# Kernel tuning notes

Measured on AMD Instinct MI355X. Metric: run time of the kernel, lower is better.

Reference implementation:

```python
import jax, jax.numpy as jnp
import numpy as np

B, L, U, H = 16, 1024, 512, 2  # batch, seq_len, units, highway_num


def setup_inputs() -> dict:
    key = jax.random.key(0)
    ks = jax.random.split(key, 8)
    s = 0.02  # weight init scale
    return {
        "inputs": jax.random.normal(ks[0], (B, L, U), dtype=jnp.float32),
        "tW": jax.random.normal(ks[1], (H, U, U), dtype=jnp.float32) * s,
        "tb": jnp.zeros((H, U), dtype=jnp.float32),
        "cW": jax.random.normal(ks[2], (H, U, U), dtype=jnp.float32) * s,
        "cb": jnp.zeros((H, U), dtype=jnp.float32),
        "aW": jax.random.normal(ks[3], (3 * U,), dtype=jnp.float32) * s,
        "ab": jnp.zeros((1,), dtype=jnp.float32),
        "frW": jax.random.normal(ks[4], (2 * U, U), dtype=jnp.float32) * s,
        "frb": jnp.zeros((U,), dtype=jnp.float32),
        "ffW": jax.random.normal(ks[5], (2 * U, U), dtype=jnp.float32) * s,
        "ffb": jnp.zeros((U,), dtype=jnp.float32),
    }


def reference(inputs, tW, tb, cW, cb, aW, ab, frW, frb, ffW, ffb):
    # Highway stack (inference: dropout is identity)
    x = inputs
    for i in range(tW.shape[0]):
        t = jax.nn.relu(x @ tW[i] + tb[i])
        c = jax.nn.sigmoid(x @ cW[i] + cb[i])
        x = t * c + x * (1.0 - c)

    # Pairwise MLP self-attention.
    # Original: A_ij = relu(dense1(concat([x_i, x_j, x_i*x_j]))).
    # Split aW = [w1; w2; w3] so we never materialize the [B,L,L,3U] tensor:
    # A_ij = relu(x_i.w1 + x_j.w2 + sum_d x_i_d * x_j_d * w3_d + b)
    u = x.shape[-1]
    w1, w2, w3 = aW[:u], aW[u:2 * u], aW[2 * u:]
    s1 = x @ w1                                    # [B,L]
    s2 = x @ w2                                    # [B,L]
    s3 = jnp.einsum('bid,bjd->bij', x * w3, x)     # [B,L,L]
    A = jax.nn.relu(s1[:, :, None] + s2[:, None, :] + s3 + ab[0])
    att = jnp.einsum('bij,bjd->bid', jax.nn.softmax(A, axis=-1), x)

    # Fuse gate. NOTE: original code uses fuse_f_dense (sigmoid) for BOTH
    # z and f (fuse_z_dense is never called), so z == f at inference.
    concat = jnp.concatenate([inputs, att], axis=-1)  # [B,L,2U]
    z = jax.nn.sigmoid(concat @ ffW + ffb)
    r = jax.nn.sigmoid(concat @ frW + frb)
    f = z
    return r * inputs + f * z
```

## Files before the change

kernel.cpp:

```cpp
#include <hip/hip_runtime.h>
#include <math.h>

typedef __bf16 bf16;
typedef __attribute__((ext_vector_type(8))) __bf16 bf16x8;
typedef __attribute__((ext_vector_type(4))) float f32x4;


__device__ __forceinline__ void load_lds16(const bf16* g, bf16* l) {
  __builtin_amdgcn_global_load_lds(
      (const __attribute__((address_space(1))) unsigned int*)(g),
      (__attribute__((address_space(3))) unsigned int*)(l), 16, 0, 0);
}

struct DualArgs {
  const bf16* A; const bf16* A2;
  const bf16* Bt;
  void* C; const void* xres;
  const float* bias_t; const float* bias_c;
  int K, ldb;
  const float* aW;
  float* s1a; float* s2a;
  bf16* q;
  bf16* xT;
};

template<int EPI>
__global__ __launch_bounds__(256, 4)
void gemm_dual(DualArgs g) {
  __shared__ bf16 smem[2 * 128 * 64];
  bf16* As = smem;
  bf16* Bs = smem + 8192;
  const int tid = threadIdx.x;
  const int bid = blockIdx.x;
  const int xcd = bid & 7;
  const int t = bid >> 3;
  const int bx = t & 7;
  const int r  = t >> 3;
  const int Rx = gridDim.x >> 6;
  const int by = xcd * Rx + r;

  const int wid = tid >> 6, lane = tid & 63;
  const int wm = (wid >> 1) << 6;
  const int wn = (wid & 1) << 6;
  const int lr = lane & 15, lq = lane >> 4;

  f32x4 acc[4][4];
#pragma unroll
  for (int i = 0; i < 4; i++)
#pragma unroll
    for (int j = 0; j < 4; j++) acc[i][j] = f32x4{0.f, 0.f, 0.f, 0.f};

  const int srow8 = (tid >> 3) & 7;
  const int skc   = (tid & 7) ^ srow8;
  const int lswz  = (lr & 7);
  const long long abase = (long long)(by * 128) * 512;

  for (int k0 = 0; k0 < g.K; k0 += 64) {
    const bf16* Ak = (k0 < 512) ? g.A : g.A2;
    const int kk = k0 & 511;
    __syncthreads();
#pragma unroll
    for (int j = 0; j < 4; j++) {
      const int ci = (tid >> 6) * 4 + j;
      const int bn = ci * 8 + srow8;
      load_lds16(Ak + abase + (long long)bn * 512 + kk + skc * 8, As + ci * 512);
      const int grp = bn >> 5, r5 = bn & 31;
      const int grow = ((grp & 1) << 9) + bx * 64 + ((grp >> 1) << 5) + r5;
      load_lds16(g.Bt + (long long)grow * g.ldb + k0 + skc * 8, Bs + ci * 512);
    }
    __syncthreads();
#pragma unroll
    for (int ks = 0; ks < 2; ks++) {
      bf16x8 af[4], bfr[4];
      const int kx = (ks * 4 + lq) ^ lswz;
#pragma unroll
      for (int i = 0; i < 4; i++)
        af[i] = *(const bf16x8*)(&As[(wm + i * 16 + lr) * 64 + kx * 8]);
#pragma unroll
      for (int j = 0; j < 4; j++)
        bfr[j] = *(const bf16x8*)(&Bs[(wn + j * 16 + lr) * 64 + kx * 8]);
#pragma unroll
      for (int i = 0; i < 4; i++)
#pragma unroll
        for (int j = 0; j < 4; j++)
          acc[i][j] = __builtin_amdgcn_mfma_f32_16x16x32_bf16(af[i], bfr[j], acc[i][j], 0, 0, 0);
    }
  }

  const int colb = bx * 64 + (wn >> 1);
  bf16 xn_arr[4][4][2];
#pragma unroll
  for (int i = 0; i < 4; i++) {
#pragma unroll
    for (int v = 0; v < 4; v++) {
      int row = by * 128 + wm + i * 16 + lq * 4 + v;
      float p1s = 0.f, p2s = 0.f;
#pragma unroll
      for (int j = 0; j < 2; j++) {
        int col = colb + j * 16 + lr;
        long long idx = (long long)row * 512 + col;
        float p0 = acc[i][j][v] + g.bias_t[col];
        float p1 = acc[i][j + 2][v] + g.bias_c[col];
        if (EPI == 1) {
          float z = 1.f / (1.f + __expf(-p0));
          float rr = 1.f / (1.f + __expf(-p1));
          float x = (float)((const bf16*)g.xres)[idx];
          ((float*)g.C)[idx] = rr * x + z * z;
        } else {
          float tt = fmaxf(p0, 0.f);
          float c = 1.f / (1.f + __expf(-p1));
          float x = (float)((const bf16*)g.xres)[idx];
          bf16 xn = (bf16)(tt * c + x * (1.f - c));
          ((bf16*)g.C)[idx] = xn;
          if (EPI == 2) {
            xn_arr[i][v][j] = xn;
            float xf = (float)xn;
            p1s += xf * g.aW[col];
            p2s += xf * g.aW[512 + col];
            g.q[idx] = (bf16)(xf * g.aW[1024 + col]);
          }
        }
      }
      if (EPI == 2) {
        p1s += __shfl_xor(p1s, 1, 64);
        p1s += __shfl_xor(p1s, 2, 64);
        p1s += __shfl_xor(p1s, 4, 64);
        p1s += __shfl_xor(p1s, 8, 64);
        p2s += __shfl_xor(p2s, 1, 64);
        p2s += __shfl_xor(p2s, 2, 64);
        p2s += __shfl_xor(p2s, 4, 64);
        p2s += __shfl_xor(p2s, 8, 64);
        if (lr == 0) {
          atomicAdd(&g.s1a[row], p1s);
          atomicAdd(&g.s2a[row], p2s);
        }
      }
    }
  }

  if (EPI == 2) {
    bf16* Ts = smem;
    __syncthreads();
#pragma unroll
    for (int i = 0; i < 4; i++)
#pragma unroll
      for (int v = 0; v < 4; v++)
#pragma unroll
        for (int j = 0; j < 2; j++) {
          int rloc = wm + i * 16 + lq * 4 + v;
          int cloc = (wn >> 1) + j * 16 + lr;
          Ts[cloc * 136 + rloc] = xn_arr[i][v][j];
        }
    __syncthreads();
    const int b = by >> 3;
    bf16* dst = g.xT + (long long)b * 524288 + ((by & 7) * 128);
#pragma unroll
    for (int it = 0; it < 2; it++) {
      int d = (tid >> 3) + it * 32;
      int jb = (tid & 7) * 16;
      bf16x8 v0 = *(const bf16x8*)(&Ts[d * 136 + jb]);
      bf16x8 v1 = *(const bf16x8*)(&Ts[d * 136 + jb + 8]);
      long long o = (long long)(bx * 64 + d) * 1024 + jb;
      *(bf16x8*)(dst + o) = v0;
      *(bf16x8*)(dst + o + 8) = v1;
    }
  }
}

struct AttnArgs {
  const bf16* Q;
  const bf16* X;
  const bf16* XT;
  bf16* O;
  const float* s1; const float* s2; const float* abp;
};

__global__ __launch_bounds__(512, 2)
void attn_fused(AttnArgs g) {
  __shared__ __align__(16) bf16 smem[57344];
  __shared__ float lsum_sh[4][64];
  bf16* Qs = smem;
  bf16* Es = smem + 49152;
  const int tid = threadIdx.x;
  const int bid = blockIdx.x;
  const int gr = (bid & 7) * 32 + (bid >> 3);
  const int bz = gr >> 4, qt = gr & 15;
  const int wid = tid >> 6, lane = tid & 63;
  const int wr = wid >> 2, wc = wid & 3;
  const int lr = lane & 15, lq = lane >> 4;
  const int lswz = lr & 7;
  const int srow8 = (lane >> 3) & 7;
  const int skc = (lane & 7) ^ srow8;

  const bf16* Qg = g.Q + (long long)bz * 524288 + (long long)(qt * 64) * 512;
  const bf16* Xg = g.X + (long long)bz * 524288;
  const bf16* XTg = g.XT + (long long)bz * 524288;

#pragma unroll
  for (int c8 = 0; c8 < 8; c8++) {
    const int row = c8 * 8 + srow8;
    load_lds16(Qg + (long long)row * 512 + wid * 64 + skc * 8,
               Qs + (wid * 8 + c8) * 512);
  }
#pragma unroll
  for (int jj = 0; jj < 2; jj++) {
    const int c = wid * 2 + jj;
    load_lds16(Xg + (long long)(c * 8 + srow8) * 512 + skc * 8,
               smem + 32768 + c * 512);
  }

  float s1r[2][4];
#pragma unroll
  for (int i = 0; i < 2; i++)
#pragma unroll
    for (int v = 0; v < 4; v++)
      s1r[i][v] = g.s1[bz * 1024 + qt * 64 + wr * 32 + i * 16 + lq * 4 + v] + g.abp[0];

  f32x4 acc_o[2][8];
  float lsum[2][4];
#pragma unroll
  for (int i = 0; i < 2; i++) {
#pragma unroll
    for (int jd = 0; jd < 8; jd++) acc_o[i][jd] = f32x4{0.f, 0.f, 0.f, 0.f};
#pragma unroll
    for (int v = 0; v < 4; v++) lsum[i][v] = 0.f;
  }

  __syncthreads();

  int cur = 0;
  for (int jt = 0; jt < 8; jt++) {
    f32x4 acc_s[2][2];
#pragma unroll
    for (int i = 0; i < 2; i++)
#pragma unroll
      for (int jjf = 0; jjf < 2; jjf++) acc_s[i][jjf] = f32x4{0.f, 0.f, 0.f, 0.f};

    for (int p = 0; p < 8; p++) {
      if (p < 7) {
#pragma unroll
        for (int jj = 0; jj < 2; jj++) {
          const int c = wid * 2 + jj;
          load_lds16(Xg + (long long)(jt * 128 + c * 8 + srow8) * 512 + (p + 1) * 64 + skc * 8,
                     smem + 32768 + (cur ^ 1) * 8192 + c * 512);
        }
      } else if (jt + 1 < 8) {
#pragma unroll
        for (int jj = 0; jj < 2; jj++) {
          const int c = wid * 2 + jj;
          load_lds16(Xg + (long long)((jt + 1) * 128 + c * 8 + srow8) * 512 + skc * 8,
                     smem + 32768 + (cur ^ 1) * 8192 + c * 512);
        }
      }
      bf16x8 aq[2][2], bx[2][2];
#pragma unroll
      for (int ks = 0; ks < 2; ks++) {
        const int kx = (ks * 4 + lq) ^ lswz;
#pragma unroll
        for (int i = 0; i < 2; i++)
          aq[i][ks] = *(const bf16x8*)(&Qs[p * 4096 + (wr * 32 + i * 16 + lr) * 64 + kx * 8]);
#pragma unroll
        for (int jjf = 0; jjf < 2; jjf++)
          bx[jjf][ks] = *(const bf16x8*)(&smem[32768 + cur * 8192 + (wc * 32 + jjf * 16 + lr) * 64 + kx * 8]);
      }
#pragma unroll
      for (int i = 0; i < 2; i++)
#pragma unroll
        for (int jjf = 0; jjf < 2; jjf++)
#pragma unroll
          for (int ks = 0; ks < 2; ks++)
            acc_s[i][jjf] = __builtin_amdgcn_mfma_f32_16x16x32_bf16(aq[i][ks], bx[jjf][ks], acc_s[i][jjf], 0, 0, 0);
      __syncthreads();
      cur ^= 1;
    }

    float s2v[2];
#pragma unroll
    for (int jjf = 0; jjf < 2; jjf++)
      s2v[jjf] = g.s2[bz * 1024 + jt * 128 + wc * 32 + jjf * 16 + lr];
#pragma unroll
    for (int i = 0; i < 2; i++) {
#pragma unroll
      for (int v = 0; v < 4; v++) {
        const int rl = wr * 32 + i * 16 + lq * 4 + v;
        float ps = 0.f;
#pragma unroll
        for (int jjf = 0; jjf < 2; jjf++) {
          const int jl = wc * 32 + jjf * 16 + lr;
          float val = acc_s[i][jjf][v] + s1r[i][v] + s2v[jjf];
          val = fminf(fmaxf(val, 0.f), 60.f);
          val = __expf(val);
          bf16 eb = (bf16)val;
          ps += (float)eb;
          Es[(jl >> 6) * 4096 + rl * 64 + (((jl >> 3) & 7) ^ (rl & 7)) * 8 + (jl & 7)] = eb;
        }
        ps += __shfl_xor(ps, 1, 64);
        ps += __shfl_xor(ps, 2, 64);
        ps += __shfl_xor(ps, 4, 64);
        ps += __shfl_xor(ps, 8, 64);
        lsum[i][v] += ps;
      }
    }
    __syncthreads();

#pragma unroll
    for (int kq = 0; kq < 4; kq++) {
      bf16x8 aE[2];
      const int kx = (((kq & 1) * 4 + lq)) ^ lswz;
#pragma unroll
      for (int i = 0; i < 2; i++)
        aE[i] = *(const bf16x8*)(&Es[(kq >> 1) * 4096 + (wr * 32 + i * 16 + lr) * 64 + kx * 8]);
      bf16x8 bv[8];
#pragma unroll
      for (int jd = 0; jd < 8; jd++)
        bv[jd] = *(const bf16x8*)(XTg + (long long)(wc * 128 + jd * 16 + lr) * 1024
                                  + jt * 128 + kq * 32 + lq * 8);
#pragma unroll
      for (int jd = 0; jd < 8; jd++) {
        acc_o[0][jd] = __builtin_amdgcn_mfma_f32_16x16x32_bf16(aE[0], bv[jd], acc_o[0][jd], 0, 0, 0);
        acc_o[1][jd] = __builtin_amdgcn_mfma_f32_16x16x32_bf16(aE[1], bv[jd], acc_o[1][jd], 0, 0, 0);
      }
    }
  }

  if (lr == 0) {
#pragma unroll
    for (int i = 0; i < 2; i++)
#pragma unroll
      for (int v = 0; v < 4; v++)
        lsum_sh[wc][wr * 32 + i * 16 + lq * 4 + v] = lsum[i][v];
  }
  __syncthreads();

  bf16* Ts = smem;
  float rinv[2][4];
#pragma unroll
  for (int i = 0; i < 2; i++)
#pragma unroll
    for (int v = 0; v < 4; v++) {
      const int rl = wr * 32 + i * 16 + lq * 4 + v;
      const float tot = lsum_sh[0][rl] + lsum_sh[1][rl] + lsum_sh[2][rl] + lsum_sh[3][rl];
      rinv[i][v] = 1.f / tot;
    }
  __syncthreads();
#pragma unroll
  for (int i = 0; i < 2; i++)
#pragma unroll
    for (int jd = 0; jd < 8; jd++)
#pragma unroll
      for (int v = 0; v < 4; v++) {
        const int rl = wr * 32 + i * 16 + lq * 4 + v;
        const int d = wc * 128 + jd * 16 + lr;
        Ts[rl * 520 + d] = (bf16)(acc_o[i][jd][v] * rinv[i][v]);
      }
  __syncthreads();
  bf16* Og = g.O + (long long)bz * 524288 + (long long)(qt * 64) * 512;
#pragma unroll
  for (int rr = 0; rr < 8; rr++) {
    const int row = wid * 8 + rr;
    bf16x8 vv = *(const bf16x8*)(&Ts[row * 520 + lane * 8]);
    *(bf16x8*)(Og + (long long)row * 512 + lane * 8) = vv;
  }
}

__device__ __forceinline__ void tile_transpose(const float* src, int sld,
                                               bf16* dst, int dld,
                                               int k0, int n0, int tid) {
  __shared__ float tile[64][65];
  const int rr = tid >> 4, c4 = (tid & 15) * 4;
#pragma unroll
  for (int it = 0; it < 4; it++) {
    int r = rr + it * 16;
    f32x4 v = *(const f32x4*)(src + (long long)(k0 + r) * sld + n0 + c4);
    tile[r][c4] = v[0]; tile[r][c4 + 1] = v[1];
    tile[r][c4 + 2] = v[2]; tile[r][c4 + 3] = v[3];
  }
  __syncthreads();
  const int nl = tid >> 2, kb = (tid & 3) * 16;
  bf16x8 o0, o1;
#pragma unroll
  for (int kk = 0; kk < 8; kk++) o0[kk] = (bf16)tile[kb + kk][nl];
#pragma unroll
  for (int kk = 0; kk < 8; kk++) o1[kk] = (bf16)tile[kb + 8 + kk][nl];
  bf16* d = dst + (long long)(n0 + nl) * dld + k0 + kb;
  *(bf16x8*)d = o0;
  *(bf16x8*)(d + 8) = o1;
}

__global__ void prep(const float* tW, const float* tb, const float* cW, const float* cb,
                     const float* frW, const float* frb, const float* ffW, const float* ffb,
                     const float* inp, bf16* xb0,
                     bf16* w1T, bf16* w2T, float* bias1, float* bias2, float* sred) {
  const int bid = blockIdx.x, tid = threadIdx.x;
  if (bid < 256) {
    const int quad = bid >> 6, tile = bid & 63;
    const int l = quad >> 1, half = quad & 1;
    const float* src = (half ? cW : tW) + l * 262144;
    bf16* dst = w1T + l * 524288 + half * 262144;
    tile_transpose(src, 512, dst, 512, (tile >> 3) * 64, (tile & 7) * 64, tid);
  } else if (bid < 512) {
    const int j = bid - 256;
    const int half = j >> 7, tile = j & 127;
    const float* src = half ? frW : ffW;
    bf16* dst = w2T + half * 524288;
    tile_transpose(src, 512, dst, 1024, (tile >> 3) * 64, (tile & 7) * 64, tid);
  } else if (bid < 4608) {
    long long i8 = (((long long)(bid - 512)) * 256 + tid) * 8;
    bf16x8 o;
#pragma unroll
    for (int k = 0; k < 8; k++) o[k] = (bf16)inp[i8 + k];
    *(bf16x8*)(xb0 + i8) = o;
  } else {
    for (int j = tid; j < 3072; j += 256) {
      if (j < 2048) {
        int l = j >> 10, n = j & 1023;
        bias1[j] = (n < 512) ? tb[l * 512 + n] : cb[l * 512 + (n - 512)];
      } else {
        int n = j - 2048;
        bias2[n] = (n < 512) ? ffb[n] : frb[n - 512];
      }
    }
    for (int j = tid; j < 12288; j += 256)
      *(f32x4*)(sred + j * 4) = f32x4{0.f, 0.f, 0.f, 0.f};
  }
}

extern "C" void kernel_launch(void* const* d_in, const int* in_sizes, int n_in,
                              void* d_out, int out_size, void* d_ws, size_t ws_size,
                              hipStream_t stream) {
  const float* inp = (const float*)d_in[0];
  const float* tW  = (const float*)d_in[1];
  const float* tb  = (const float*)d_in[2];
  const float* cW  = (const float*)d_in[3];
  const float* cb  = (const float*)d_in[4];
  const float* aW  = (const float*)d_in[5];
  const float* ab  = (const float*)d_in[6];
  const float* frW = (const float*)d_in[7];
  const float* frb = (const float*)d_in[8];
  const float* ffW = (const float*)d_in[9];
  const float* ffb = (const float*)d_in[10];
  float* out = (float*)d_out;

  char* p = (char*)d_ws;
  auto alloc = [&](size_t bytes) { char* r = p; p += (bytes + 255) & ~size_t(255); return r; };
  bf16* xb0   = (bf16*) alloc(16777216);
  bf16* x1    = (bf16*) alloc(16777216);
  bf16* x2    = (bf16*) alloc(16777216);
  bf16* q16   = (bf16*) alloc(16777216);
  bf16* xT16  = (bf16*) alloc(16777216);
  bf16* att16 = (bf16*) alloc(16777216);
  float* sred = (float*)alloc(196608);
  bf16* w1T   = (bf16*) alloc(2097152);
  bf16* w2T   = (bf16*) alloc(2097152);
  float* bias1= (float*)alloc(8192);
  float* bias2= (float*)alloc(4096);
  float* s1 = sred, *s2 = sred + 16384;

  prep<<<4609, 256, 0, stream>>>(
      tW, tb, cW, cb, frW, frb, ffW, ffb, inp, xb0, w1T, w2T, bias1, bias2, sred);

  {
    DualArgs g{};
    g.A = xb0; g.A2 = xb0; g.Bt = w1T;
    g.C = x1; g.xres = xb0;
    g.bias_t = bias1; g.bias_c = bias1 + 512;
    g.K = 512; g.ldb = 512;
    gemm_dual<0><<<1024, 256, 0, stream>>>(g);
  }
  {
    DualArgs g{};
    g.A = x1; g.A2 = x1; g.Bt = w1T + 524288;
    g.C = x2; g.xres = x1;
    g.bias_t = bias1 + 1024; g.bias_c = bias1 + 1536;
    g.K = 512; g.ldb = 512;
    g.aW = aW; g.s1a = s1; g.s2a = s2; g.q = q16; g.xT = xT16;
    gemm_dual<2><<<1024, 256, 0, stream>>>(g);
  }
  {
    AttnArgs g{};
    g.Q = q16; g.X = x2; g.XT = xT16; g.O = att16;
    g.s1 = s1; g.s2 = s2; g.abp = ab;
    attn_fused<<<256, 512, 0, stream>>>(g);
  }
  {
    DualArgs g{};
    g.A = xb0; g.A2 = att16; g.Bt = w2T;
    g.C = out; g.xres = xb0;
    g.bias_t = bias2; g.bias_c = bias2 + 512;
    g.K = 1024; g.ldb = 1024;
    gemm_dual<1><<<1024, 256, 0, stream>>>(g);
  }
}
```

Baseline: 322.6 us.

## Store Q, X and X^T in MFMA fragment order and load attention operands directly

The second highway GEMM epilogue now writes x2, q and the transposed x in a pre-swizzled per-lane fragment layout through LDS staging, with q computed from the staged tile. The attention kernel then loads MFMA operands straight from global memory with coalesced per-lane 16-byte loads. This removes the Q/X LDS staging, the double-buffered global-to-LDS pipeline and its per-step barriers, and shrinks LDS so more blocks can be resident. The cost is that the operands are now read directly from global/L2 without software prefetch, which may expose load latency, and the epilogue does extra LDS passes.

```diff
diff --git a/kernel.cpp b/kernel.cpp
--- a/kernel.cpp
+++ b/kernel.cpp
@@ -111,13 +111,12 @@
           float c = 1.f / (1.f + __expf(-p1));
           float x = (float)((const bf16*)g.xres)[idx];
           bf16 xn = (bf16)(tt * c + x * (1.f - c));
-          ((bf16*)g.C)[idx] = xn;
+          if (EPI == 0) ((bf16*)g.C)[idx] = xn;
           if (EPI == 2) {
             xn_arr[i][v][j] = xn;
             float xf = (float)xn;
             p1s += xf * g.aW[col];
             p2s += xf * g.aW[512 + col];
-            g.q[idx] = (bf16)(xf * g.aW[1024 + col]);
           }
         }
       }
@@ -139,6 +138,8 @@
   }
 
   if (EPI == 2) {
+    const int l15 = lane & 15, l4 = lane >> 4;
+    const long long bb = (long long)(by >> 3) * 524288;
     bf16* Ts = smem;
     __syncthreads();
 #pragma unroll
@@ -152,35 +153,66 @@
           Ts[cloc * 136 + rloc] = xn_arr[i][v][j];
         }
     __syncthreads();
-    const int b = by >> 3;
-    bf16* dst = g.xT + (long long)b * 524288 + ((by & 7) * 128);
-#pragma unroll
-    for (int it = 0; it < 2; it++) {
-      int d = (tid >> 3) + it * 32;
-      int jb = (tid & 7) * 16;
-      bf16x8 v0 = *(const bf16x8*)(&Ts[d * 136 + jb]);
-      bf16x8 v1 = *(const bf16x8*)(&Ts[d * 136 + jb + 8]);
-      long long o = (long long)(bx * 64 + d) * 1024 + jb;
-      *(bf16x8*)(dst + o) = v0;
-      *(bf16x8*)(dst + o + 8) = v1;
+    {
+      bf16* xtf = g.xT + bb;
+#pragma unroll
+      for (int f = 0; f < 4; f++) {
+        const int id = wid * 4 + f;
+        const int Dl = id >> 2, Jl = id & 3;
+        bf16x8 v = *(const bf16x8*)(&Ts[(Dl * 16 + l15) * 136 + Jl * 32 + l4 * 8]);
+        const int D = bx * 4 + Dl, J = (by & 7) * 4 + Jl;
+        *(bf16x8*)(xtf + ((long long)(D * 32 + J) * 64 + lane) * 8) = v;
+      }
+    }
+    __syncthreads();
+    bf16* Ts2 = smem;
+#pragma unroll
+    for (int i = 0; i < 4; i++)
+#pragma unroll
+      for (int v = 0; v < 4; v++)
+#pragma unroll
+        for (int j = 0; j < 2; j++) {
+          int rloc = wm + i * 16 + lq * 4 + v;
+          int cloc = (wn >> 1) + j * 16 + lr;
+          Ts2[rloc * 72 + cloc] = xn_arr[i][v][j];
+        }
+    __syncthreads();
+    {
+      bf16* qf = g.q + bb;
+      bf16* xf = (bf16*)g.C + bb;
+#pragma unroll
+      for (int f = 0; f < 4; f++) {
+        const int id = wid * 4 + f;
+        const int Rl = id >> 1, Pl = id & 1;
+        bf16x8 v = *(const bf16x8*)(&Ts2[(Rl * 16 + l15) * 72 + Pl * 32 + l4 * 8]);
+        const long long o = ((long long)(((by & 7) * 8 + Rl) * 16 + (bx * 2 + Pl)) * 64 + lane) * 8;
+        *(bf16x8*)(xf + o) = v;
+        const float* aw = g.aW + 1024 + bx * 64 + Pl * 32 + l4 * 8;
+        f32x4 w0 = *(const f32x4*)aw;
+        f32x4 w1 = *(const f32x4*)(aw + 4);
+        bf16x8 qv;
+#pragma unroll
+        for (int k = 0; k < 4; k++) qv[k] = (bf16)((float)v[k] * w0[k]);
+#pragma unroll
+        for (int k = 0; k < 4; k++) qv[4 + k] = (bf16)((float)v[4 + k] * w1[k]);
+        *(bf16x8*)(qf + o) = qv;
+      }
     }
   }
 }
 
 struct AttnArgs {
-  const bf16* Q;
-  const bf16* X;
-  const bf16* XT;
+  const bf16* Qf;
+  const bf16* Xf;
+  const bf16* XTf;
   bf16* O;
   const float* s1; const float* s2; const float* abp;
 };
 
 __global__ __launch_bounds__(512, 2)
 void attn_fused(AttnArgs g) {
-  __shared__ __align__(16) bf16 smem[57344];
+  __shared__ __align__(16) bf16 smem[33280];
   __shared__ float lsum_sh[4][64];
-  bf16* Qs = smem;
-  bf16* Es = smem + 49152;
   const int tid = threadIdx.x;
   const int bid = blockIdx.x;
   const int gr = (bid & 7) * 32 + (bid >> 3);
@@ -188,26 +220,10 @@
   const int wid = tid >> 6, lane = tid & 63;
   const int wr = wid >> 2, wc = wid & 3;
   const int lr = lane & 15, lq = lane >> 4;
-  const int lswz = lr & 7;
-  const int srow8 = (lane >> 3) & 7;
-  const int skc = (lane & 7) ^ srow8;
-
-  const bf16* Qg = g.Q + (long long)bz * 524288 + (long long)(qt * 64) * 512;
-  const bf16* Xg = g.X + (long long)bz * 524288;
-  const bf16* XTg = g.XT + (long long)bz * 524288;
-
-#pragma unroll
-  for (int c8 = 0; c8 < 8; c8++) {
-    const int row = c8 * 8 + srow8;
-    load_lds16(Qg + (long long)row * 512 + wid * 64 + skc * 8,
-               Qs + (wid * 8 + c8) * 512);
-  }
-#pragma unroll
-  for (int jj = 0; jj < 2; jj++) {
-    const int c = wid * 2 + jj;
-    load_lds16(Xg + (long long)(c * 8 + srow8) * 512 + skc * 8,
-               smem + 32768 + c * 512);
-  }
+
+  const bf16* Qf  = g.Qf  + (long long)bz * 524288;
+  const bf16* Xf  = g.Xf  + (long long)bz * 524288;
+  const bf16* XTf = g.XTf + (long long)bz * 524288;
 
   float s1r[2][4];
 #pragma unroll
@@ -226,9 +242,6 @@
     for (int v = 0; v < 4; v++) lsum[i][v] = 0.f;
   }
 
-  __syncthreads();
-
-  int cur = 0;
   for (int jt = 0; jt < 8; jt++) {
     f32x4 acc_s[2][2];
 #pragma unroll
@@ -236,44 +249,23 @@
 #pragma unroll
       for (int jjf = 0; jjf < 2; jjf++) acc_s[i][jjf] = f32x4{0.f, 0.f, 0.f, 0.f};
 
+#pragma unroll
     for (int p = 0; p < 8; p++) {
-      if (p < 7) {
-#pragma unroll
-        for (int jj = 0; jj < 2; jj++) {
-          const int c = wid * 2 + jj;
-          load_lds16(Xg + (long long)(jt * 128 + c * 8 + srow8) * 512 + (p + 1) * 64 + skc * 8,
-                     smem + 32768 + (cur ^ 1) * 8192 + c * 512);
-        }
-      } else if (jt + 1 < 8) {
-#pragma unroll
-        for (int jj = 0; jj < 2; jj++) {
-          const int c = wid * 2 + jj;
-          load_lds16(Xg + (long long)((jt + 1) * 128 + c * 8 + srow8) * 512 + skc * 8,
-                     smem + 32768 + (cur ^ 1) * 8192 + c * 512);
-        }
-      }
-      bf16x8 aq[2][2], bx[2][2];
 #pragma unroll
       for (int ks = 0; ks < 2; ks++) {
-        const int kx = (ks * 4 + lq) ^ lswz;
-#pragma unroll
-        for (int i = 0; i < 2; i++)
-          aq[i][ks] = *(const bf16x8*)(&Qs[p * 4096 + (wr * 32 + i * 16 + lr) * 64 + kx * 8]);
-#pragma unroll
-        for (int jjf = 0; jjf < 2; jjf++)
-          bx[jjf][ks] = *(const bf16x8*)(&smem[32768 + cur * 8192 + (wc * 32 + jjf * 16 + lr) * 64 + kx * 8]);
-      }
-#pragma unroll
-      for (int i = 0; i < 2; i++)
-#pragma unroll
-        for (int jjf = 0; jjf < 2; jjf++)
-#pragma unroll
-          for (int ks = 0; ks < 2; ks++)
-            acc_s[i][jjf] = __builtin_amdgcn_mfma_f32_16x16x32_bf16(aq[i][ks], bx[jjf][ks], acc_s[i][jjf], 0, 0, 0);
-      __syncthreads();
-      cur ^= 1;
-    }
-
+        const int P = p * 2 + ks;
+        bf16x8 aq0 = *(const bf16x8*)(Qf + (((qt * 4 + wr * 2 + 0) * 16 + P) * 64 + lane) * 8);
+        bf16x8 aq1 = *(const bf16x8*)(Qf + (((qt * 4 + wr * 2 + 1) * 16 + P) * 64 + lane) * 8);
+        bf16x8 b0  = *(const bf16x8*)(Xf + (((jt * 8 + wc * 2 + 0) * 16 + P) * 64 + lane) * 8);
+        bf16x8 b1  = *(const bf16x8*)(Xf + (((jt * 8 + wc * 2 + 1) * 16 + P) * 64 + lane) * 8);
+        acc_s[0][0] = __builtin_amdgcn_mfma_f32_16x16x32_bf16(aq0, b0, acc_s[0][0], 0, 0, 0);
+        acc_s[0][1] = __builtin_amdgcn_mfma_f32_16x16x32_bf16(aq0, b1, acc_s[0][1], 0, 0, 0);
+        acc_s[1][0] = __builtin_amdgcn_mfma_f32_16x16x32_bf16(aq1, b0, acc_s[1][0], 0, 0, 0);
+        acc_s[1][1] = __builtin_amdgcn_mfma_f32_16x16x32_bf16(aq1, b1, acc_s[1][1], 0, 0, 0);
+      }
+    }
+
+    if (jt) __syncthreads();
     float s2v[2];
 #pragma unroll
     for (int jjf = 0; jjf < 2; jjf++)
@@ -292,7 +284,7 @@
           val = __expf(val);
           bf16 eb = (bf16)val;
           ps += (float)eb;
-          Es[(jl >> 6) * 4096 + rl * 64 + (((jl >> 3) & 7) ^ (rl & 7)) * 8 + (jl & 7)] = eb;
+          smem[(jl >> 6) * 4096 + rl * 64 + (((jl >> 3) & 7) ^ (rl & 7)) * 8 + (jl & 7)] = eb;
         }
         ps += __shfl_xor(ps, 1, 64);
         ps += __shfl_xor(ps, 2, 64);
@@ -306,19 +298,16 @@
 #pragma unroll
     for (int kq = 0; kq < 4; kq++) {
       bf16x8 aE[2];
-      const int kx = (((kq & 1) * 4 + lq)) ^ lswz;
-#pragma unroll
-      for (int i = 0; i < 2; i++)
-        aE[i] = *(const bf16x8*)(&Es[(kq >> 1) * 4096 + (wr * 32 + i * 16 + lr) * 64 + kx * 8]);
-      bf16x8 bv[8];
-#pragma unroll
-      for (int jd = 0; jd < 8; jd++)
-        bv[jd] = *(const bf16x8*)(XTg + (long long)(wc * 128 + jd * 16 + lr) * 1024
-                                  + jt * 128 + kq * 32 + lq * 8);
+#pragma unroll
+      for (int i = 0; i < 2; i++) {
+        const int row = wr * 32 + i * 16 + lr;
+        aE[i] = *(const bf16x8*)(&smem[(kq >> 1) * 4096 + row * 64 + ((((kq & 1) * 4 + lq) ^ (row & 7)) * 8)]);
+      }
 #pragma unroll
       for (int jd = 0; jd < 8; jd++) {
-        acc_o[0][jd] = __builtin_amdgcn_mfma_f32_16x16x32_bf16(aE[0], bv[jd], acc_o[0][jd], 0, 0, 0);
-        acc_o[1][jd] = __builtin_amdgcn_mfma_f32_16x16x32_bf16(aE[1], bv[jd], acc_o[1][jd], 0, 0, 0);
+        bf16x8 bv = *(const bf16x8*)(XTf + (((wc * 8 + jd) * 32 + jt * 4 + kq) * 64 + lane) * 8);
+        acc_o[0][jd] = __builtin_amdgcn_mfma_f32_16x16x32_bf16(aE[0], bv, acc_o[0][jd], 0, 0, 0);
+        acc_o[1][jd] = __builtin_amdgcn_mfma_f32_16x16x32_bf16(aE[1], bv, acc_o[1][jd], 0, 0, 0);
       }
     }
   }
@@ -332,17 +321,16 @@
   }
   __syncthreads();
 
-  bf16* Ts = smem;
   float rinv[2][4];
 #pragma unroll
   for (int i = 0; i < 2; i++)
 #pragma unroll
     for (int v = 0; v < 4; v++) {
       const int rl = wr * 32 + i * 16 + lq * 4 + v;
-      const float tot = lsum_sh[0][rl] + lsum_sh[1][rl] + lsum_sh[2][rl] + lsum_sh[3][rl];
-      rinv[i][v] = 1.f / tot;
-    }
-  __syncthreads();
+      rinv[i][v] = 1.f / (lsum_sh[0][rl] + lsum_sh[1][rl] + lsum_sh[2][rl] + lsum_sh[3][rl]);
+    }
+
+  bf16* Ts = smem;
 #pragma unroll
   for (int i = 0; i < 2; i++)
 #pragma unroll
@@ -355,11 +343,14 @@
       }
   __syncthreads();
   bf16* Og = g.O + (long long)bz * 524288 + (long long)(qt * 64) * 512;
-#pragma unroll
-  for (int rr = 0; rr < 8; rr++) {
-    const int row = wid * 8 + rr;
-    bf16x8 vv = *(const bf16x8*)(&Ts[row * 520 + lane * 8]);
-    *(bf16x8*)(Og + (long long)row * 512 + lane * 8) = vv;
+  {
+    const int row = tid >> 3;
+    const int c8 = (tid & 7) * 8;
+#pragma unroll
+    for (int it = 0; it < 8; it++) {
+      const int col = c8 + it * 64;
+      *(bf16x8*)(Og + (long long)row * 512 + col) = *(const bf16x8*)(&Ts[row * 520 + col]);
+    }
   }
 }
 
@@ -445,9 +436,9 @@
   auto alloc = [&](size_t bytes) { char* r = p; p += (bytes + 255) & ~size_t(255); return r; };
   bf16* xb0   = (bf16*) alloc(16777216);
   bf16* x1    = (bf16*) alloc(16777216);
-  bf16* x2    = (bf16*) alloc(16777216);
-  bf16* q16   = (bf16*) alloc(16777216);
-  bf16* xT16  = (bf16*) alloc(16777216);
+  bf16* x2f   = (bf16*) alloc(16777216);
+  bf16* q16f  = (bf16*) alloc(16777216);
+  bf16* xTf   = (bf16*) alloc(16777216);
   bf16* att16 = (bf16*) alloc(16777216);
   float* sred = (float*)alloc(196608);
   bf16* w1T   = (bf16*) alloc(2097152);
@@ -470,15 +461,15 @@
   {
     DualArgs g{};
     g.A = x1; g.A2 = x1; g.Bt = w1T + 524288;
-    g.C = x2; g.xres = x1;
+    g.C = x2f; g.xres = x1;
     g.bias_t = bias1 + 1024; g.bias_c = bias1 + 1536;
     g.K = 512; g.ldb = 512;
-    g.aW = aW; g.s1a = s1; g.s2a = s2; g.q = q16; g.xT = xT16;
+    g.aW = aW; g.s1a = s1; g.s2a = s2; g.q = q16f; g.xT = xTf;
     gemm_dual<2><<<1024, 256, 0, stream>>>(g);
   }
   {
     AttnArgs g{};
-    g.Q = q16; g.X = x2; g.XT = xT16; g.O = att16;
+    g.Qf = q16f; g.Xf = x2f; g.XTf = xTf; g.O = att16;
     g.s1 = s1; g.s2 = s2; g.abp = ab;
     attn_fused<<<256, 512, 0, stream>>>(g);
   }
```

New measurement: 341.0 us. 1.06x slower.
